# Optimization experiments

Hardware: AMD Instinct MI355X
Metric: run time of the kernel (lower is better)

## Reference

```python
import jax, jax.numpy as jnp
import numpy as np

NF, GC, K, B, H, W = 64, 64, 8, 16, 96, 96
CINS = [NF, NF + GC, NF + 2 * GC, NF + 3 * GC, NF + 4 * GC]


def _dynconv(x, w, b, aw1, ab1, aw2, ab2):
    # x:[B,C,H,W]  w:[K,O,C,3,3]  b:[K,O]
    # CondConv-style attention: GAP -> fc -> relu -> fc -> softmax (temperature=1)
    pooled = x.mean(axis=(2, 3))                       # [B,C]
    h = jax.nn.relu(pooled @ aw1.T + ab1)              # [B,hid]
    attn = jax.nn.softmax(h @ aw2.T + ab2, axis=-1)    # [B,K]
    wk = jnp.einsum('bk,koihw->boihw', attn, w)        # per-sample kernels [B,O,C,3,3]
    bk = attn @ b                                      # [B,O]
    conv1 = lambda xi, wi: jax.lax.conv_general_dilated(
        xi[None], wi, (1, 1), ((1, 1), (1, 1)),
        dimension_numbers=('NCHW', 'OIHW', 'NCHW'))[0]
    return jax.vmap(conv1)(x, wk) + bk[:, :, None, None]


def _lrelu(v):
    return jnp.where(v >= 0, v, 0.2 * v)


def _forward(x, params):
    x1 = _lrelu(_dynconv(x, *params[0]))
    x2 = _lrelu(_dynconv(jnp.concatenate([x, x1], 1), *params[1]))
    x3 = _lrelu(_dynconv(jnp.concatenate([x, x1, x2], 1), *params[2]))
    x4 = _lrelu(_dynconv(jnp.concatenate([x, x1, x2, x3], 1), *params[3]))
    x5 = _dynconv(jnp.concatenate([x, x1, x2, x3, x4], 1), *params[4])
    return x5 * 0.2 + x


def setup_inputs() -> dict:
    key = jax.random.key(0)
    ks = iter(jax.random.split(key, 64))
    inp = {"x": jax.random.normal(next(ks), (B, NF, H, W), jnp.float32)}
    for i, cin in enumerate(CINS, 1):
        hid = cin // 4
        inp[f"w{i}"] = jax.random.normal(next(ks), (K, GC, cin, 3, 3), jnp.float32) * 0.05
        inp[f"b{i}"] = jnp.zeros((K, GC), jnp.float32)
        inp[f"aw1_{i}"] = jax.random.normal(next(ks), (hid, cin), jnp.float32) * 0.05
        inp[f"ab1_{i}"] = jnp.zeros((hid,), jnp.float32)
        inp[f"aw2_{i}"] = jax.random.normal(next(ks), (K, hid), jnp.float32) * 0.05
        inp[f"ab2_{i}"] = jnp.zeros((K,), jnp.float32)
    return inp


def reference(x, w1, b1, aw1_1, ab1_1, aw2_1, ab2_1,
              w2, b2, aw1_2, ab1_2, aw2_2, ab2_2,
              w3, b3, aw1_3, ab1_3, aw2_3, ab2_3,
              w4, b4, aw1_4, ab1_4, aw2_4, ab2_4,
              w5, b5, aw1_5, ab1_5, aw2_5, ab2_5):
    params = [(w1, b1, aw1_1, ab1_1, aw2_1, ab2_1),
              (w2, b2, aw1_2, ab1_2, aw2_2, ab2_2),
              (w3, b3, aw1_3, ab1_3, aw2_3, ab2_3),
              (w4, b4, aw1_4, ab1_4, aw2_4, ab2_4),
              (w5, b5, aw1_5, ab1_5, aw2_5, ab2_5)]
    return _forward(x, params)
```

## Files before the change

kernel.cpp:

```cpp
#include <hip/hip_runtime.h>

#define HW 9216

typedef __bf16 bf16x8 __attribute__((ext_vector_type(8)));
typedef float  f32x4  __attribute__((ext_vector_type(4)));
typedef unsigned short u16;

__global__ void pooled_kernel(const float* __restrict__ src, int b_stride, int ch_base,
                              float* __restrict__ pooled, int pout_base) {
    int b = blockIdx.x >> 6;
    int c = blockIdx.x & 63;
    const float4* p4 = (const float4*)(src + ((size_t)b * b_stride + ch_base + c) * HW);
    float s = 0.f;
    for (int i = threadIdx.x; i < HW / 4; i += 256) {
        float4 v = p4[i];
        s += (v.x + v.y) + (v.z + v.w);
    }
    for (int off = 32; off; off >>= 1) s += __shfl_down(s, off, 64);
    __shared__ float red[4];
    int lane = threadIdx.x & 63, wid = threadIdx.x >> 6;
    if (!lane) red[wid] = s;
    __syncthreads();
    if (!threadIdx.x)
        pooled[b * 320 + pout_base + c] = (red[0] + red[1] + red[2] + red[3]) * (1.0f / HW);
}

__global__ void attn_kernel(const float* __restrict__ pooled,
                            const float* __restrict__ aw1, const float* __restrict__ ab1,
                            const float* __restrict__ aw2, const float* __restrict__ ab2,
                            const float* __restrict__ bconst,
                            float* __restrict__ attn, float* __restrict__ bk,
                            int cin, int hid) {
    int b = blockIdx.x;
    int t = threadIdx.x;
    __shared__ float sp[320];
    __shared__ float sh[80];
    __shared__ float sl[8];
    __shared__ float sa[8];
    for (int c = t; c < cin; c += 128) sp[c] = pooled[b * 320 + c];
    __syncthreads();
    if (t < hid) {
        float acc = ab1[t];
        const float* row = aw1 + (size_t)t * cin;
        for (int c = 0; c < cin; ++c) acc = fmaf(row[c], sp[c], acc);
        sh[t] = acc > 0.f ? acc : 0.f;
    }
    __syncthreads();
    if (t < 8) {
        float acc = ab2[t];
        const float* row = aw2 + t * hid;
        for (int j = 0; j < hid; ++j) acc = fmaf(row[j], sh[j], acc);
        sl[t] = acc;
    }
    __syncthreads();
    if (t == 0) {
        float m = sl[0];
        for (int k = 1; k < 8; ++k) m = fmaxf(m, sl[k]);
        float e[8], ssum = 0.f;
        for (int k = 0; k < 8; ++k) { e[k] = expf(sl[k] - m); ssum += e[k]; }
        float inv = 1.0f / ssum;
        for (int k = 0; k < 8; ++k) { sa[k] = e[k] * inv; attn[b * 8 + k] = sa[k]; }
    }
    __syncthreads();
    if (t < 64) {
        float acc = 0.f;
        for (int k = 0; k < 8; ++k) acc = fmaf(sa[k], bconst[k * 64 + t], acc);
        bk[b * 64 + t] = acc;
    }
}

__global__ __launch_bounds__(256)
void pack_weights(const float* __restrict__ w, const float* __restrict__ attn,
                  u16* __restrict__ PWH, u16* __restrict__ PWL, int cin) {
    __shared__ float sa[128];
    int t = threadIdx.x;
    if (t < 128) sa[t] = attn[t];
    __syncthreads();
    int g = blockIdx.x * 256 + t;
    int nch = cin >> 5;
    if (g >= nch * 2304) return;
    int oc = g & 63;
    int r = g >> 6;
    int kg = r & 3;
    int ct = r >> 2;
    int tap = ct % 9;
    int chunk = ct / 9;
    int c0 = chunk * 32 + kg * 8;
    float wv[8][8];
#pragma unroll
    for (int k = 0; k < 8; ++k)
#pragma unroll
        for (int i = 0; i < 8; ++i)
            wv[k][i] = w[(((size_t)k * 64 + oc) * cin + c0 + i) * 9 + tap];
#pragma unroll 1
    for (int b = 0; b < 16; ++b) {
        bf16x8 Hv, Lv;
#pragma unroll
        for (int i = 0; i < 8; ++i) {
            float v = 0.f;
#pragma unroll
            for (int k = 0; k < 8; ++k) v = fmaf(sa[b * 8 + k], wv[k][i], v);
            __bf16 hh = (__bf16)v;
            float rr = v - (float)hh;
            Hv[i] = hh;
            Lv[i] = (__bf16)rr;
        }
        size_t base = ((size_t)(b * nch + chunk) * 9 + tap) * 2048 + kg * 512 + oc * 8;
        *(bf16x8*)(PWH + base) = Hv;
        *(bf16x8*)(PWL + base) = Lv;
    }
}

template <int CIN, bool FINAL>
__global__ __launch_bounds__(256, 2)
void conv_mfma(const float* __restrict__ x, const float* __restrict__ Fq,
               const u16* __restrict__ PWH, const u16* __restrict__ PWL,
               const float* __restrict__ bk, float* __restrict__ out, int OB)
{
    constexpr int NCHK = CIN / 32;
    const int b  = blockIdx.y;
    const int h0 = blockIdx.x * 2;
    const int t  = threadIdx.x;
    const int w  = t >> 6;
    const int l  = t & 63;
    const int l15 = l & 15;
    const int l4  = l >> 4;
    const int orow  = w >> 1;
    const int ocol0 = (w & 1) * 48;

    __shared__ bf16x8 sX[2][1600];

    f32x4 acc[4][3];
#pragma unroll
    for (int q = 0; q < 4; ++q)
#pragma unroll
        for (int pf = 0; pf < 3; ++pf) acc[q][pf] = (f32x4){0.f, 0.f, 0.f, 0.f};

    const int aoff = l4 * 512 + l15 * 8;

#pragma unroll 1
    for (int chunk = 0; chunk < NCHK; ++chunk) {
        __syncthreads();
        const int c0 = chunk * 32;
        for (int s = l; s < 392; s += 64) {
            int row = s / 98;
            int col = s - row * 98;
            int rin = h0 - 1 + row;
            int ci  = col - 1;
            bool ok = ((unsigned)rin < 96u) && ((unsigned)ci < 96u);
            int off = rin * 96 + ci;
            bf16x8 Hv, Lv;
#pragma unroll
            for (int i = 0; i < 8; ++i) {
                int cg = c0 + w * 8 + i;
                const float* bp = (cg < 64)
                    ? (x + ((size_t)b * 64 + cg) * HW)
                    : (Fq + ((size_t)b * 256 + (cg - 64)) * HW);
                float v = ok ? bp[off] : 0.f;
                __bf16 hh = (__bf16)v;
                float rr = v - (float)hh;
                Hv[i] = hh;
                Lv[i] = (__bf16)rr;
            }
            int S = (w ^ (col & 3) ^ ((col >> 2) & 3)) & 3;
            int slot = (row * 100 + col) * 4 + S;
            sX[0][slot] = Hv;
            sX[1][slot] = Lv;
        }
        __syncthreads();

        const u16* pwh = PWH + ((size_t)(b * NCHK + chunk) * 9) * 2048 + aoff;
        const u16* pwl = PWL + ((size_t)(b * NCHK + chunk) * 9) * 2048 + aoff;
#pragma unroll
        for (int tap = 0; tap < 9; ++tap) {
            const int kh = tap / 3, kw = tap % 3;
            bf16x8 Ah[4], Al[4];
#pragma unroll
            for (int q = 0; q < 4; ++q) {
                Ah[q] = *(const bf16x8*)(pwh + tap * 2048 + q * 128);
                Al[q] = *(const bf16x8*)(pwl + tap * 2048 + q * 128);
            }
#pragma unroll
            for (int pf = 0; pf < 3; ++pf) {
                int col = ocol0 + pf * 16 + l15 + kw;
                int row = orow + kh;
                int S = (l4 ^ (col & 3) ^ ((col >> 2) & 3)) & 3;
                int slot = (row * 100 + col) * 4 + S;
                bf16x8 Bh = sX[0][slot];
                bf16x8 Bl = sX[1][slot];
#pragma unroll
                for (int q = 0; q < 4; ++q) {
                    acc[q][pf] = __builtin_amdgcn_mfma_f32_16x16x32_bf16(Ah[q], Bh, acc[q][pf], 0, 0, 0);
                    acc[q][pf] = __builtin_amdgcn_mfma_f32_16x16x32_bf16(Ah[q], Bl, acc[q][pf], 0, 0, 0);
                    acc[q][pf] = __builtin_amdgcn_mfma_f32_16x16x32_bf16(Al[q], Bh, acc[q][pf], 0, 0, 0);
                }
            }
        }
    }

    const int orow_g = h0 + orow;
#pragma unroll
    for (int q = 0; q < 4; ++q) {
#pragma unroll
        for (int rg = 0; rg < 4; ++rg) {
            int oc = q * 16 + l4 * 4 + rg;
            float bias = bk[b * 64 + oc];
            float* op = out + ((size_t)b * OB + oc) * HW + orow_g * 96;
#pragma unroll
            for (int pf = 0; pf < 3; ++pf) {
                int cc = ocol0 + pf * 16 + l15;
                float v = acc[q][pf][rg] + bias;
                if (FINAL) {
                    const float* xp = x + ((size_t)b * 64 + oc) * HW + orow_g * 96;
                    op[cc] = 0.2f * v + xp[cc];
                } else {
                    op[cc] = (v >= 0.f) ? v : 0.2f * v;
                }
            }
        }
    }
}

extern "C" void kernel_launch(void* const* d_in, const int* in_sizes, int n_in,
                              void* d_out, int out_size, void* d_ws, size_t ws_size,
                              hipStream_t stream) {
    const float* x = (const float*)d_in[0];
    float* out = (float*)d_out;

    float* F = (float*)d_ws;
    u16* PWH = (u16*)(F + (size_t)16 * 256 * HW);
    u16* PWL = PWH + (size_t)16 * 10 * 9 * 2048;
    float* pooled = (float*)(PWL + (size_t)16 * 10 * 9 * 2048);
    float* attn = pooled + 16 * 320;
    float* bk = attn + 16 * 8;

    const int cins[5] = {64, 128, 192, 256, 320};
    dim3 cgrid(48, 16);

    for (int li = 0; li < 5; ++li) {
        const float* w   = (const float*)d_in[1 + li * 6 + 0];
        const float* bb  = (const float*)d_in[1 + li * 6 + 1];
        const float* aw1 = (const float*)d_in[1 + li * 6 + 2];
        const float* ab1 = (const float*)d_in[1 + li * 6 + 3];
        const float* aw2 = (const float*)d_in[1 + li * 6 + 4];
        const float* ab2 = (const float*)d_in[1 + li * 6 + 5];
        const int cin = cins[li];
        const int hid = cin / 4;
        const int nch = cin / 32;

        if (li == 0)
            pooled_kernel<<<dim3(16 * 64), 256, 0, stream>>>(x, 64, 0, pooled, 0);
        else
            pooled_kernel<<<dim3(16 * 64), 256, 0, stream>>>(F, 256, (li - 1) * 64, pooled, li * 64);

        attn_kernel<<<dim3(16), 128, 0, stream>>>(pooled, aw1, ab1, aw2, ab2, bb,
                                                  attn, bk, cin, hid);

        pack_weights<<<dim3(9 * nch), 256, 0, stream>>>(w, attn, PWH, PWL, cin);

        switch (li) {
            case 0: conv_mfma< 64, false><<<cgrid, 256, 0, stream>>>(x, F, PWH, PWL, bk, F + (size_t)0 * 64 * HW, 256); break;
            case 1: conv_mfma<128, false><<<cgrid, 256, 0, stream>>>(x, F, PWH, PWL, bk, F + (size_t)1 * 64 * HW, 256); break;
            case 2: conv_mfma<192, false><<<cgrid, 256, 0, stream>>>(x, F, PWH, PWL, bk, F + (size_t)2 * 64 * HW, 256); break;
            case 3: conv_mfma<256, false><<<cgrid, 256, 0, stream>>>(x, F, PWH, PWL, bk, F + (size_t)3 * 64 * HW, 256); break;
            case 4: conv_mfma<320, true ><<<cgrid, 256, 0, stream>>>(x, F, PWH, PWL, bk, out, 64); break;
        }
    }
}
```

Before: 778.4 us.

## Store activations pre-split as packed bf16 hi/lo and prefetch next chunk

Input and intermediate features are now stored in a channel-group-interleaved layout of 8 bf16 values, already split into high and low halves. A split_x pre-pass and the conv epilogues write this layout, so the conv tile load becomes vectorized 16-byte loads instead of eight strided fp32 gathers plus per-element conversion. The next channel chunk is also prefetched into registers during the MFMA loop, overlapping global loads with compute. Pooling for later layers reads the packed format. The cost is extra workspace, more register pressure from the prefetch buffers, and reconstructing values from bf16 hi+lo pairs.

```diff
diff --git a/kernel.cpp b/kernel.cpp
--- a/kernel.cpp
+++ b/kernel.cpp
@@ -3,14 +3,33 @@
 #define HW 9216
 
 typedef __bf16 bf16x8 __attribute__((ext_vector_type(8)));
+typedef __bf16 bf16x4 __attribute__((ext_vector_type(4)));
 typedef float  f32x4  __attribute__((ext_vector_type(4)));
 typedef unsigned short u16;
 
-__global__ void pooled_kernel(const float* __restrict__ src, int b_stride, int ch_base,
-                              float* __restrict__ pooled, int pout_base) {
+__global__ void split_x(const float* __restrict__ x, u16* __restrict__ PKH,
+                        u16* __restrict__ PKL) {
+    int b = blockIdx.x >> 3, g = blockIdx.x & 7;
+    for (int px = threadIdx.x; px < HW; px += 256) {
+        bf16x8 Hv, Lv;
+#pragma unroll
+        for (int i = 0; i < 8; ++i) {
+            float v = x[((size_t)b * 64 + g * 8 + i) * HW + px];
+            __bf16 hh = (__bf16)v;
+            Hv[i] = hh;
+            Lv[i] = (__bf16)(v - (float)hh);
+        }
+        size_t base = ((size_t)(b * 40 + g) * HW + px) * 8;
+        *(bf16x8*)(PKH + base) = Hv;
+        *(bf16x8*)(PKL + base) = Lv;
+    }
+}
+
+__global__ void pooled_kernel(const float* __restrict__ src,
+                              float* __restrict__ pooled) {
     int b = blockIdx.x >> 6;
     int c = blockIdx.x & 63;
-    const float4* p4 = (const float4*)(src + ((size_t)b * b_stride + ch_base + c) * HW);
+    const float4* p4 = (const float4*)(src + ((size_t)b * 64 + c) * HW);
     float s = 0.f;
     for (int i = threadIdx.x; i < HW / 4; i += 256) {
         float4 v = p4[i];
@@ -22,7 +41,38 @@
     if (!lane) red[wid] = s;
     __syncthreads();
     if (!threadIdx.x)
-        pooled[b * 320 + pout_base + c] = (red[0] + red[1] + red[2] + red[3]) * (1.0f / HW);
+        pooled[b * 320 + c] = (red[0] + red[1] + red[2] + red[3]) * (1.0f / HW);
+}
+
+__global__ void pooled_pk(const u16* __restrict__ PKH, const u16* __restrict__ PKL,
+                          float* __restrict__ pooled, int gbase, int pbase) {
+    int b = blockIdx.x >> 3, gr = blockIdx.x & 7;
+    const u16* bh = PKH + ((size_t)(b * 40 + gbase + gr) * HW) * 8;
+    const u16* bl = PKL + ((size_t)(b * 40 + gbase + gr) * HW) * 8;
+    float acc[8];
+#pragma unroll
+    for (int i = 0; i < 8; ++i) acc[i] = 0.f;
+    for (int px = threadIdx.x; px < HW; px += 256) {
+        bf16x8 H = *(const bf16x8*)(bh + px * 8);
+        bf16x8 L = *(const bf16x8*)(bl + px * 8);
+#pragma unroll
+        for (int i = 0; i < 8; ++i) acc[i] += (float)H[i] + (float)L[i];
+    }
+#pragma unroll
+    for (int i = 0; i < 8; ++i)
+        for (int off = 32; off; off >>= 1) acc[i] += __shfl_down(acc[i], off, 64);
+    __shared__ float red[4][8];
+    int lane = threadIdx.x & 63, wid = threadIdx.x >> 6;
+    if (!lane) {
+#pragma unroll
+        for (int i = 0; i < 8; ++i) red[wid][i] = acc[i];
+    }
+    __syncthreads();
+    if (threadIdx.x < 8) {
+        float s = red[0][threadIdx.x] + red[1][threadIdx.x] +
+                  red[2][threadIdx.x] + red[3][threadIdx.x];
+        pooled[b * 320 + pbase + gr * 8 + threadIdx.x] = s * (1.0f / HW);
+    }
 }
 
 __global__ void attn_kernel(const float* __restrict__ pooled,
@@ -101,9 +151,8 @@
 #pragma unroll
             for (int k = 0; k < 8; ++k) v = fmaf(sa[b * 8 + k], wv[k][i], v);
             __bf16 hh = (__bf16)v;
-            float rr = v - (float)hh;
             Hv[i] = hh;
-            Lv[i] = (__bf16)rr;
+            Lv[i] = (__bf16)(v - (float)hh);
         }
         size_t base = ((size_t)(b * nch + chunk) * 9 + tap) * 2048 + kg * 512 + oc * 8;
         *(bf16x8*)(PWH + base) = Hv;
@@ -113,9 +162,10 @@
 
 template <int CIN, bool FINAL>
 __global__ __launch_bounds__(256, 2)
-void conv_mfma(const float* __restrict__ x, const float* __restrict__ Fq,
-               const u16* __restrict__ PWH, const u16* __restrict__ PWL,
-               const float* __restrict__ bk, float* __restrict__ out, int OB)
+void conv_mfma(const float* __restrict__ x, u16* __restrict__ PKH,
+               u16* __restrict__ PKL, const u16* __restrict__ PWH,
+               const u16* __restrict__ PWL, const float* __restrict__ bk,
+               float* __restrict__ out, int ogbase)
 {
     constexpr int NCHK = CIN / 32;
     const int b  = blockIdx.y;
@@ -136,38 +186,63 @@
 #pragma unroll
         for (int pf = 0; pf < 3; ++pf) acc[q][pf] = (f32x4){0.f, 0.f, 0.f, 0.f};
 
+    bf16x8 zv;
+#pragma unroll
+    for (int i = 0; i < 8; ++i) zv[i] = (__bf16)0.f;
+
+    bf16x8 ph[7], pl[7];
+
     const int aoff = l4 * 512 + l15 * 8;
+
+    {
+        int gg = 0 * 4 + w;
+        const u16* bh = PKH + ((size_t)(b * 40 + gg) * HW) * 8;
+        const u16* bl = PKL + ((size_t)(b * 40 + gg) * HW) * 8;
+#pragma unroll
+        for (int j = 0; j < 7; ++j) {
+            int s = l + 64 * j;
+            if (s < 392) {
+                int row = s / 98, col = s - row * 98;
+                int rin = h0 - 1 + row, ci = col - 1;
+                bool ok = ((unsigned)rin < 96u) && ((unsigned)ci < 96u);
+                size_t off = (size_t)(rin * 96 + ci) * 8;
+                ph[j] = ok ? *(const bf16x8*)(bh + off) : zv;
+                pl[j] = ok ? *(const bf16x8*)(bl + off) : zv;
+            }
+        }
+    }
+#pragma unroll
+    for (int j = 0; j < 7; ++j) {
+        int s = l + 64 * j;
+        if (s < 392) {
+            int row = s / 98, col = s - row * 98;
+            int S = (w ^ (col & 3) ^ ((col >> 2) & 3)) & 3;
+            int slot = (row * 100 + col) * 4 + S;
+            sX[0][slot] = ph[j];
+            sX[1][slot] = pl[j];
+        }
+    }
+    __syncthreads();
 
 #pragma unroll 1
     for (int chunk = 0; chunk < NCHK; ++chunk) {
-        __syncthreads();
-        const int c0 = chunk * 32;
-        for (int s = l; s < 392; s += 64) {
-            int row = s / 98;
-            int col = s - row * 98;
-            int rin = h0 - 1 + row;
-            int ci  = col - 1;
-            bool ok = ((unsigned)rin < 96u) && ((unsigned)ci < 96u);
-            int off = rin * 96 + ci;
-            bf16x8 Hv, Lv;
-#pragma unroll
-            for (int i = 0; i < 8; ++i) {
-                int cg = c0 + w * 8 + i;
-                const float* bp = (cg < 64)
-                    ? (x + ((size_t)b * 64 + cg) * HW)
-                    : (Fq + ((size_t)b * 256 + (cg - 64)) * HW);
-                float v = ok ? bp[off] : 0.f;
-                __bf16 hh = (__bf16)v;
-                float rr = v - (float)hh;
-                Hv[i] = hh;
-                Lv[i] = (__bf16)rr;
-            }
-            int S = (w ^ (col & 3) ^ ((col >> 2) & 3)) & 3;
-            int slot = (row * 100 + col) * 4 + S;
-            sX[0][slot] = Hv;
-            sX[1][slot] = Lv;
-        }
-        __syncthreads();
+        if (chunk + 1 < NCHK) {
+            int gg = (chunk + 1) * 4 + w;
+            const u16* bh = PKH + ((size_t)(b * 40 + gg) * HW) * 8;
+            const u16* bl = PKL + ((size_t)(b * 40 + gg) * HW) * 8;
+#pragma unroll
+            for (int j = 0; j < 7; ++j) {
+                int s = l + 64 * j;
+                if (s < 392) {
+                    int row = s / 98, col = s - row * 98;
+                    int rin = h0 - 1 + row, ci = col - 1;
+                    bool ok = ((unsigned)rin < 96u) && ((unsigned)ci < 96u);
+                    size_t off = (size_t)(rin * 96 + ci) * 8;
+                    ph[j] = ok ? *(const bf16x8*)(bh + off) : zv;
+                    pl[j] = ok ? *(const bf16x8*)(bl + off) : zv;
+                }
+            }
+        }
 
         const u16* pwh = PWH + ((size_t)(b * NCHK + chunk) * 9) * 2048 + aoff;
         const u16* pwl = PWL + ((size_t)(b * NCHK + chunk) * 9) * 2048 + aoff;
@@ -196,26 +271,60 @@
                 }
             }
         }
+
+        __syncthreads();
+        if (chunk + 1 < NCHK) {
+#pragma unroll
+            for (int j = 0; j < 7; ++j) {
+                int s = l + 64 * j;
+                if (s < 392) {
+                    int row = s / 98, col = s - row * 98;
+                    int S = (w ^ (col & 3) ^ ((col >> 2) & 3)) & 3;
+                    int slot = (row * 100 + col) * 4 + S;
+                    sX[0][slot] = ph[j];
+                    sX[1][slot] = pl[j];
+                }
+            }
+            __syncthreads();
+        }
     }
 
     const int orow_g = h0 + orow;
 #pragma unroll
     for (int q = 0; q < 4; ++q) {
-#pragma unroll
-        for (int rg = 0; rg < 4; ++rg) {
-            int oc = q * 16 + l4 * 4 + rg;
-            float bias = bk[b * 64 + oc];
-            float* op = out + ((size_t)b * OB + oc) * HW + orow_g * 96;
+        if (FINAL) {
+#pragma unroll
+            for (int rg = 0; rg < 4; ++rg) {
+                int oc = q * 16 + l4 * 4 + rg;
+                float bias = bk[b * 64 + oc];
+                float* op = out + ((size_t)b * 64 + oc) * HW + orow_g * 96;
+                const float* xp = x + ((size_t)b * 64 + oc) * HW + orow_g * 96;
+#pragma unroll
+                for (int pf = 0; pf < 3; ++pf) {
+                    int cc = ocol0 + pf * 16 + l15;
+                    float v = acc[q][pf][rg] + bias;
+                    op[cc] = 0.2f * v + xp[cc];
+                }
+            }
+        } else {
+            const int go = ogbase + 2 * q + (l4 >> 1);
+            const int ib = (l4 & 1) * 4;
 #pragma unroll
             for (int pf = 0; pf < 3; ++pf) {
                 int cc = ocol0 + pf * 16 + l15;
-                float v = acc[q][pf][rg] + bias;
-                if (FINAL) {
-                    const float* xp = x + ((size_t)b * 64 + oc) * HW + orow_g * 96;
-                    op[cc] = 0.2f * v + xp[cc];
-                } else {
-                    op[cc] = (v >= 0.f) ? v : 0.2f * v;
-                }
+                bf16x4 hv, lv;
+#pragma unroll
+                for (int rg = 0; rg < 4; ++rg) {
+                    int oc = q * 16 + l4 * 4 + rg;
+                    float v = acc[q][pf][rg] + bk[b * 64 + oc];
+                    v = (v >= 0.f) ? v : 0.2f * v;
+                    __bf16 hh = (__bf16)v;
+                    hv[rg] = hh;
+                    lv[rg] = (__bf16)(v - (float)hh);
+                }
+                size_t base = ((size_t)(b * 40 + go) * HW + orow_g * 96 + cc) * 8 + ib;
+                *(bf16x4*)(PKH + base) = hv;
+                *(bf16x4*)(PKL + base) = lv;
             }
         }
     }
@@ -227,8 +336,9 @@
     const float* x = (const float*)d_in[0];
     float* out = (float*)d_out;
 
-    float* F = (float*)d_ws;
-    u16* PWH = (u16*)(F + (size_t)16 * 256 * HW);
+    u16* PKH = (u16*)d_ws;
+    u16* PKL = PKH + (size_t)16 * 40 * HW * 8;
+    u16* PWH = PKL + (size_t)16 * 40 * HW * 8;
     u16* PWL = PWH + (size_t)16 * 10 * 9 * 2048;
     float* pooled = (float*)(PWL + (size_t)16 * 10 * 9 * 2048);
     float* attn = pooled + 16 * 320;
@@ -236,6 +346,8 @@
 
     const int cins[5] = {64, 128, 192, 256, 320};
     dim3 cgrid(48, 16);
+
+    split_x<<<dim3(128), 256, 0, stream>>>(x, PKH, PKL);
 
     for (int li = 0; li < 5; ++li) {
         const float* w   = (const float*)d_in[1 + li * 6 + 0];
@@ -249,21 +361,23 @@
         const int nch = cin / 32;
 
         if (li == 0)
-            pooled_kernel<<<dim3(16 * 64), 256, 0, stream>>>(x, 64, 0, pooled, 0);
+            pooled_kernel<<<dim3(16 * 64), 256, 0, stream>>>(x, pooled);
         else
-            pooled_kernel<<<dim3(16 * 64), 256, 0, stream>>>(F, 256, (li - 1) * 64, pooled, li * 64);
+            pooled_pk<<<dim3(128), 256, 0, stream>>>(PKH, PKL, pooled,
+                                                     8 + 8 * (li - 1), li * 64);
 
         attn_kernel<<<dim3(16), 128, 0, stream>>>(pooled, aw1, ab1, aw2, ab2, bb,
                                                   attn, bk, cin, hid);
 
         pack_weights<<<dim3(9 * nch), 256, 0, stream>>>(w, attn, PWH, PWL, cin);
 
+        const int ogbase = 8 + 8 * li;
         switch (li) {
-            case 0: conv_mfma< 64, false><<<cgrid, 256, 0, stream>>>(x, F, PWH, PWL, bk, F + (size_t)0 * 64 * HW, 256); break;
-            case 1: conv_mfma<128, false><<<cgrid, 256, 0, stream>>>(x, F, PWH, PWL, bk, F + (size_t)1 * 64 * HW, 256); break;
-            case 2: conv_mfma<192, false><<<cgrid, 256, 0, stream>>>(x, F, PWH, PWL, bk, F + (size_t)2 * 64 * HW, 256); break;
-            case 3: conv_mfma<256, false><<<cgrid, 256, 0, stream>>>(x, F, PWH, PWL, bk, F + (size_t)3 * 64 * HW, 256); break;
-            case 4: conv_mfma<320, true ><<<cgrid, 256, 0, stream>>>(x, F, PWH, PWL, bk, out, 64); break;
-        }
-    }
-}
+            case 0: conv_mfma< 64, false><<<cgrid, 256, 0, stream>>>(x, PKH, PKL, PWH, PWL, bk, out, ogbase); break;
+            case 1: conv_mfma<128, false><<<cgrid, 256, 0, stream>>>(x, PKH, PKL, PWH, PWL, bk, out, ogbase); break;
+            case 2: conv_mfma<192, false><<<cgrid, 256, 0, stream>>>(x, PKH, PKL, PWH, PWL, bk, out, ogbase); break;
+            case 3: conv_mfma<256, false><<<cgrid, 256, 0, stream>>>(x, PKH, PKL, PWH, PWL, bk, out, ogbase); break;
+            case 4: conv_mfma<320, true ><<<cgrid, 256, 0, stream>>>(x, PKH, PKL, PWH, PWL, bk, out, ogbase); break;
+        }
+    }
+}
```

Measured after the change: 984.8 us. 26.5% more time.
